# Kernel tuning notes

Hardware: AMD Instinct MI355X
Metric: run time of the kernel (lower is better)

## Reference

```python
import jax, jax.numpy as jnp
import numpy as np

PHI = 0.1  # fraction of pruned weights randomized per inference


def setup_inputs() -> dict:
    key = jax.random.key(0)
    k1, k2, k3 = jax.random.split(key, 3)
    d_out, d_in, batch = 8192, 8192, 256
    W = jax.random.normal(k1, (d_out, d_in), jnp.float32) * 0.02
    prune = jax.random.uniform(k2, (d_out, d_in)) < 0.9
    W = jnp.where(prune, 0.0, W)
    mask = (W == 0.0)  # _register_masks: pruned positions
    x = jax.random.normal(k3, (batch, d_in), jnp.float32)
    return {"x": x, "W": W, "mask": mask}


def reference(x, W, mask):
    # --- _apply_random_flip (vectorized) ---
    n_pruned = int(np.asarray(jnp.sum(mask)))          # concrete mask -> static count
    n_flip = max(1, int(PHI * n_pruned))
    keep = ~mask
    n_keep = jnp.sum(keep).astype(W.dtype)
    wk = jnp.where(keep, W, 0.0)
    mean = jnp.sum(wk) / n_keep
    # torch .std() is unbiased (n-1 denominator)
    var = jnp.sum(jnp.where(keep, (W - mean) ** 2, 0.0)) / (n_keep - 1.0)
    std = jnp.sqrt(var)
    key = jax.random.key(42)
    ks, kv = jax.random.split(key)
    # uniform random permutation of pruned indices -> top_k of random scores
    scores = jnp.where(mask.ravel(), jax.random.uniform(ks, (W.size,)), -1.0)
    _, flip_idx = jax.lax.top_k(scores, n_flip)        # [n_flip] flat indices into W
    vals = jax.random.normal(kv, (n_flip,), W.dtype) * std * 0.1
    W_flipped = W.ravel().at[flip_idx].set(vals).reshape(W.shape)
    # --- base_model forward (Linear, no bias) ---
    out = x @ W_flipped.T                               # [batch, d_out]
    # --- _restore_masks: zero flipped weights again (no effect on out) ---
    _ = jnp.where(mask, 0.0, W_flipped)
    return out
```

## Files before the change

### kernel.cpp

```cpp
#include <hip/hip_runtime.h>

typedef unsigned int u32;
typedef unsigned long long u64;
typedef unsigned short u16;

#define NTOT   67108864u
#define T0P    7543296u
#define PBASE  14733u
#define NSUP   1651u
#define NWSEG  4096u
#define WCAP   2176u
#define RCAP   4352u
#define KSPLIT 8
#define RBLK   512u
#define SEGPB  8

struct Scalars {
  double sumW;
  double sumW2;
  u64 npruned;
  u64 nflip;
  float stdf;
  float pad;
};

#define OFF_COLSUM 0ull
#define OFF_SBASE  8192ull
#define OFF_SC     16384ull
#define OFF_SEGCNT 16512ull
#define OFF_XBF    33024ull
#define OFF_SEGS   4227328ull
#define OFF_ROUTED 39878912ull
#define OFF_WBF    75530496ull
#define WS_NEED_WBF 209748224ull
#define OFF_OUTP   OFF_SEGS

__host__ __device__ inline void tf2x32(u32 k0, u32 k1, u32 x0, u32 x1, u32& y0, u32& y1) {
  u32 ks2 = k0 ^ k1 ^ 0x1BD11BDAu;
  x0 += k0; x1 += k1;
#define TFR(r) { x0 += x1; x1 = (x1 << (r)) | (x1 >> (32 - (r))); x1 ^= x0; }
  TFR(13) TFR(15) TFR(26) TFR(6)  x0 += k1;  x1 += ks2 + 1u;
  TFR(17) TFR(29) TFR(16) TFR(24) x0 += ks2; x1 += k0 + 2u;
  TFR(13) TFR(15) TFR(26) TFR(6)  x0 += k0;  x1 += k1 + 3u;
  TFR(17) TFR(29) TFR(16) TFR(24) x0 += k1;  x1 += ks2 + 4u;
  TFR(13) TFR(15) TFR(26) TFR(6)  x0 += ks2; x1 += k0 + 5u;
#undef TFR
  y0 = x0; y1 = x1;
}

__device__ inline u32 jax_bits32(u32 k0, u32 k1, u32 i) {
  u32 y0, y1; tf2x32(k0, k1, 0u, i, y0, y1);
  return y0 ^ y1;
}

__device__ inline u16 f2bf(float f) {
  union { float f; u32 u; } c; c.f = f;
  u32 r = ((c.u >> 16) & 1u) + 0x7FFFu;
  return (u16)((c.u + r) >> 16);
}

__device__ inline float erfinv32(float x) {
  float w = -log1pf(-x * x);
  float p;
  if (w < 5.0f) {
    w -= 2.5f;
    p = 2.81022636e-08f;
    p = fmaf(p, w, 3.43273939e-07f);
    p = fmaf(p, w, -3.5233877e-06f);
    p = fmaf(p, w, -4.39150654e-06f);
    p = fmaf(p, w, 0.00021858087f);
    p = fmaf(p, w, -0.00125372503f);
    p = fmaf(p, w, -0.00417768164f);
    p = fmaf(p, w, 0.246640727f);
    p = fmaf(p, w, 1.50140941f);
  } else {
    w = sqrtf(w) - 3.0f;
    p = -0.000200214257f;
    p = fmaf(p, w, 0.000100950558f);
    p = fmaf(p, w, 0.00134934322f);
    p = fmaf(p, w, -0.00367342844f);
    p = fmaf(p, w, 0.00573950773f);
    p = fmaf(p, w, -0.0076224613f);
    p = fmaf(p, w, 0.00943887047f);
    p = fmaf(p, w, 1.00167406f);
    p = fmaf(p, w, 2.83297682f);
  }
  return p * x;
}

__global__ __launch_bounds__(256) void k_pass1w(const float* __restrict__ W,
                                                u16* __restrict__ wbf,
                                                const float* __restrict__ x,
                                                u16* __restrict__ xbf,
                                                Scalars* sc, u32* segcnt, u32* segs,
                                                u32 uk0, u32 uk1, u32 dowbf) {
  u32 t = threadIdx.x;
  u32 bid = blockIdx.x;
  if (bid < 1024u) {
    u32 gid = bid * 256 + t;
    u32 lane = t & 63;
    u32 wid = gid >> 6;
    u32* wseg = segs + (u64)wid * WCAP;
    u32 wbase = 0;
    float sf = 0.f, sf2 = 0.f; u32 cnt = 0;
    const u32 stride4 = 1024u * 256u * 4u;
    for (u32 b4 = gid * 4; b4 < NTOT; b4 += stride4) {
      float4 w4 = *(const float4*)(W + b4);
      u32 sb0 = jax_bits32(uk0, uk1, b4 + 0) >> 9;
      u32 sb1 = jax_bits32(uk0, uk1, b4 + 1) >> 9;
      u32 sb2 = jax_bits32(uk0, uk1, b4 + 2) >> 9;
      u32 sb3 = jax_bits32(uk0, uk1, b4 + 3) >> 9;
      float we[4] = {w4.x, w4.y, w4.z, w4.w};
      u32 sbv[4] = {sb0, sb1, sb2, sb3};
      u32 cand[4]; u32 nc = 0;
#pragma unroll
      for (int e = 0; e < 4; e++) {
        float w = we[e];
        sf += w;
        sf2 = fmaf(w, w, sf2);
        bool pr = (w == 0.0f);
        cnt += pr ? 1u : 0u;
        if (pr && sbv[e] >= T0P) { cand[nc] = b4 + e; nc++; }
      }
      u32 inc = nc;
#pragma unroll
      for (int o = 1; o < 64; o <<= 1) { u32 v = (u32)__shfl_up((int)inc, o); if (lane >= (u32)o) inc += v; }
      u32 tot = (u32)__shfl((int)inc, 63);
      u32 pos = wbase + inc - nc;
      for (u32 k2 = 0; k2 < nc; k2++)
        if (pos + k2 < WCAP) wseg[pos + k2] = cand[k2];
      wbase += tot;
    }
    double s = (double)sf, s2 = (double)sf2;
    for (int o = 32; o > 0; o >>= 1) {
      s += __shfl_down(s, o); s2 += __shfl_down(s2, o); cnt += __shfl_down(cnt, o);
    }
    if (lane == 0) {
      atomicAdd(&sc->sumW, s);
      atomicAdd(&sc->sumW2, s2);
      atomicAdd(&sc->npruned, (u64)cnt);
      segcnt[wid] = (wbase > WCAP) ? WCAP : wbase;
    }
  } else if (bid < 1984u) {
    if (!dowbf) return;
    u32 i0 = (bid - 1024u) * 256 + t;
    const u32 stride = 960u * 256u;
    for (u32 g = i0; g < NTOT / 8u; g += stride) {
      const float4* p = (const float4*)(W + (u64)g * 8);
      float4 a = p[0], b = p[1];
      uint4 o;
      o.x = (u32)f2bf(a.x) | ((u32)f2bf(a.y) << 16);
      o.y = (u32)f2bf(a.z) | ((u32)f2bf(a.w) << 16);
      o.z = (u32)f2bf(b.x) | ((u32)f2bf(b.y) << 16);
      o.w = (u32)f2bf(b.z) | ((u32)f2bf(b.w) << 16);
      *(uint4*)(wbf + (u64)g * 8) = o;
    }
  } else {
    u32 i0 = (bid - 1984u) * 256 + t;
    const u32 stride = 64u * 256u;
    for (u32 g = i0; g < 524288u; g += stride) {
      float4 v = ((const float4*)x)[g];
      ushort4 o; o.x = f2bf(v.x); o.y = f2bf(v.y); o.z = f2bf(v.z); o.w = f2bf(v.w);
      ((ushort4*)xbf)[g] = o;
    }
  }
}

__global__ __launch_bounds__(256) void k_route(const u32* __restrict__ segs,
                                               const u32* __restrict__ segcnt,
                                               u32* gcur, u32* routed,
                                               u32 uk0, u32 uk1) {
  __shared__ u32 lhist[2048];
  __shared__ u32 lbase[2048];
  u32 t = threadIdx.x;
  for (u32 j = t; j < 2048; j += 256) lhist[j] = 0;
  __syncthreads();
#pragma unroll 1
  for (int sg = 0; sg < SEGPB; sg++) {
    u32 wid = blockIdx.x * SEGPB + sg;
    u32 n = segcnt[wid]; if (n > WCAP) n = WCAP;
    const u32* sp = segs + (u64)wid * WCAP;
    for (u32 i = t; i < n; i += 256)
      atomicAdd(&lhist[(jax_bits32(uk0, uk1, sp[i]) >> 18) - PBASE], 1u);
  }
  __syncthreads();
  for (u32 j = t; j < 2048; j += 256) {
    u32 c = lhist[j];
    lbase[j] = c ? atomicAdd(&gcur[j], c) : 0u;
    lhist[j] = 0;
  }
  __syncthreads();
#pragma unroll 1
  for (int sg = 0; sg < SEGPB; sg++) {
    u32 wid = blockIdx.x * SEGPB + sg;
    u32 n = segcnt[wid]; if (n > WCAP) n = WCAP;
    const u32* sp = segs + (u64)wid * WCAP;
    for (u32 i = t; i < n; i += 256) {
      u32 idx = sp[i];
      u32 sup = (jax_bits32(uk0, uk1, idx) >> 18) - PBASE;
      u32 pos = lbase[sup] + atomicAdd(&lhist[sup], 1u);
      if (pos < RCAP) routed[(u64)sup * RCAP + pos] = idx;
    }
  }
}

__global__ __launch_bounds__(256) void k_scan(const u32* __restrict__ colsum, Scalars* sc,
                                              u32* sbase) {
  __shared__ u32 h[2048];
  __shared__ u32 wtmp[4];
  u32 t = threadIdx.x, lane = t & 63, wv = t >> 6;
  for (u32 j = t; j < 2048; j += 256) h[j] = colsum[j];
  __syncthreads();
  u32 a[8]; u32 s8 = 0;
#pragma unroll
  for (int k = 0; k < 8; k++) { a[k] = h[2047 - (t * 8 + k)]; s8 += a[k]; }
  u32 inc = s8;
#pragma unroll
  for (int o = 1; o < 64; o <<= 1) { u32 v = (u32)__shfl_up((int)inc, o); if (lane >= (u32)o) inc += v; }
  if (lane == 63) wtmp[wv] = inc;
  __syncthreads();
  u32 woff = 0; for (u32 w = 0; w < wv; w++) woff += wtmp[w];
  u32 base = woff + inc - s8;
#pragma unroll
  for (int k = 0; k < 8; k++) { sbase[2047 - (t * 8 + k)] = base; base += a[k]; }
  if (t == 0) {
    double nk = (double)NTOT - (double)sc->npruned;
    double mean = sc->sumW / nk;
    double var = (sc->sumW2 - 2.0 * mean * sc->sumW + nk * mean * mean) / (nk - 1.0);
    sc->stdf = (float)sqrt(var);
    u64 nfi = (u64)(0.1 * (double)sc->npruned);
    if (nfi < 1) nfi = 1;
    sc->nflip = nfi;
  }
}

__device__ inline void suf512(const u32* cnt, u32* suf, u32* wtmp) {
  u32 t = threadIdx.x, lane = t & 63, wv = t >> 6;
  u32 a0 = cnt[511 - t * 2], a1 = cnt[510 - t * 2];
  u32 s = a0 + a1;
  u32 inc = s;
#pragma unroll
  for (int o = 1; o < 64; o <<= 1) { u32 v = (u32)__shfl_up((int)inc, o); if (lane >= (u32)o) inc += v; }
  if (lane == 63) wtmp[wv] = inc;
  __syncthreads();
  u32 woff = 0;
  for (u32 w = 0; w < wv; w++) woff += wtmp[w];
  u32 base = woff + inc - s;
  suf[511 - t * 2] = base;
  suf[510 - t * 2] = base + a0;
  __syncthreads();
}

template<int MODE>
__global__ __launch_bounds__(256) void k_rank(float* __restrict__ W,
                                              u16* __restrict__ wbf,
                                              const u32* __restrict__ colsum,
                                              const u32* __restrict__ sbase,
                                              const u32* __restrict__ routed,
                                              const Scalars* __restrict__ sc,
                                              u32 uk0, u32 uk1, u32 vk0, u32 vk1) {
  u32 p = blockIdx.x;
  u32 n = colsum[p]; if (n == 0) return;
  if (n > RCAP) n = RCAP;
  u64 nflip = sc->nflip;
  u32 rbase = sbase[p];
  if ((u64)rbase >= nflip) return;
  __shared__ u32 sIdx[RCAP];
  __shared__ u16 sFine[RCAP];
  __shared__ u32 pIdx[RCAP];
  __shared__ u32 hist[512], gbase[512], cur[512], wtmp[4];
  u32 t = threadIdx.x;
  for (u32 j = t; j < 512; j += 256) hist[j] = 0;
  __syncthreads();
  const u32* src = routed + (u64)p * RCAP;
  for (u32 i = t; i < n; i += 256) {
    u32 idx = src[i];
    u32 f = (jax_bits32(uk0, uk1, idx) >> 9) & 511u;
    sIdx[i] = idx;
    sFine[i] = (u16)f;
    atomicAdd(&hist[f], 1u);
  }
  __syncthreads();
  suf512(hist, gbase, wtmp);
  for (u32 j = t; j < 512; j += 256) cur[j] = gbase[j];
  __syncthreads();
  for (u32 i = t; i < n; i += 256) {
    u32 pos = atomicAdd(&cur[sFine[i]], 1u);
    pIdx[pos] = sIdx[i];
  }
  __syncthreads();
  float stdf = sc->stdf;
  for (u32 i = t; i < n; i += 256) {
    u32 f = sFine[i];
    u32 g0 = gbase[f], g1 = g0 + hist[f];
    u32 v = sIdx[i];
    u32 ord = 0;
    for (u32 q = g0; q < g1; q++) ord += (pIdx[q] < v) ? 1u : 0u;
    u64 rank = (u64)rbase + g0 + ord;
    if (rank >= nflip) continue;
    u32 bits = jax_bits32(vk0, vk1, (u32)rank);
    union { u32 u; float fl; } cv; cv.u = 0x3F800000u | (bits >> 9);
    float fu = cv.fl - 1.0f;
    const float lo = -0.99999994f;
    float u2 = fmaxf(lo, fu * 2.0f + lo);
    float nrm = 1.41421354f * erfinv32(u2);
    float val = (nrm * stdf) * 0.1f;
    if (MODE == 1) wbf[v] = f2bf(val);
    else           W[v] = val;
  }
}

typedef __bf16 bf16x8 __attribute__((ext_vector_type(8)));
typedef float f32x4 __attribute__((ext_vector_type(4)));

__global__ __launch_bounds__(256, 3) void k_gemm2(const u16* __restrict__ xbf,
                                                  const u16* __restrict__ wbf,
                                                  float* __restrict__ outp) {
  __shared__ u16 As[128 * 64];
  __shared__ u16 Bs[128 * 64];
  u32 i = blockIdx.x;
  u32 xcd = i & 7u, slot = i >> 3;
  u32 mi = slot & 1u, qq = slot >> 1;
  u32 pid = xcd * 64u + qq;
  u32 kidx = pid >> 6;
  u32 nb = pid & 63u;
  u32 mrow = mi * 128u, nrow = nb * 128u;
  u32 kbase = kidx * 1024u;
  u32 tid = threadIdx.x;
  u32 lane = tid & 63, wv = tid >> 6;
  u32 l8 = lane & 7;
  u32 lr = lane >> 3;
  u32 wm = wv >> 1, wn = wv & 1;
  u32 r = lane & 15, q = lane >> 4;
  f32x4 acc[4][4];
#pragma unroll
  for (int a = 0; a < 4; a++)
#pragma unroll
    for (int b = 0; b < 4; b++) acc[a][b] = (f32x4){0.f, 0.f, 0.f, 0.f};

  for (u32 kb = kbase; kb < kbase + 1024u; kb += 64u) {
#pragma unroll
    for (int j = 0; j < 4; j++) {
      u32 g = wv * 4 + (u32)j;
      u32 row = g * 8 + lr;
      u32 sc = ((l8 ^ (row & 7u)) * 8u);
      const u16* ga = xbf + (u64)(mrow + row) * 8192 + kb + sc;
      __builtin_amdgcn_global_load_lds((const u32*)ga, (u32*)&As[g * 512u], 16, 0, 0);
      const u16* gb = wbf + (u64)(nrow + row) * 8192 + kb + sc;
      __builtin_amdgcn_global_load_lds((const u32*)gb, (u32*)&Bs[g * 512u], 16, 0, 0);
    }
    __syncthreads();
#pragma unroll
    for (int ks = 0; ks < 2; ks++) {
      bf16x8 a[4], b[4];
      u32 ch = (u32)(ks * 4) + q;
#pragma unroll
      for (int mt = 0; mt < 4; mt++) {
        u32 row = wm * 64 + (u32)mt * 16 + r;
        a[mt] = *(bf16x8*)&As[row * 64 + ((ch ^ (r & 7u)) * 8u)];
      }
#pragma unroll
      for (int nt = 0; nt < 4; nt++) {
        u32 row = wn * 64 + (u32)nt * 16 + r;
        b[nt] = *(bf16x8*)&Bs[row * 64 + ((ch ^ (r & 7u)) * 8u)];
      }
#pragma unroll
      for (int mt = 0; mt < 4; mt++)
#pragma unroll
        for (int nt = 0; nt < 4; nt++)
          acc[mt][nt] = __builtin_amdgcn_mfma_f32_16x16x32_bf16(a[mt], b[nt], acc[mt][nt], 0, 0, 0);
    }
    __syncthreads();
  }
  float* op = outp + (u64)kidx * 2097152u;
  u32 quad = lane >> 4, col = lane & 15;
#pragma unroll
  for (int mt = 0; mt < 4; mt++)
#pragma unroll
    for (int nt = 0; nt < 4; nt++) {
      u32 n = nrow + wn * 64 + (u32)nt * 16 + col;
#pragma unroll
      for (int rg = 0; rg < 4; rg++) {
        u32 m = mrow + wm * 64 + (u32)mt * 16 + quad * 4 + (u32)rg;
        op[(u64)m * 8192 + n] = acc[mt][nt][rg];
      }
    }
}

__global__ __launch_bounds__(256) void k_redout(const float* __restrict__ part,
                                                float* __restrict__ out) {
  u32 i = blockIdx.x * 256 + threadIdx.x;
  float4 s = ((const float4*)part)[i];
#pragma unroll
  for (int k = 1; k < KSPLIT; k++) {
    float4 v = ((const float4*)(part + (u64)k * 2097152u))[i];
    s.x += v.x; s.y += v.y; s.z += v.z; s.w += v.w;
  }
  ((float4*)out)[i] = s;
}

__global__ __launch_bounds__(256, 2) void k_gemm_fb(const u16* __restrict__ xbf,
                                                    const float* __restrict__ W,
                                                    float* __restrict__ out) {
  __shared__ u16 xs[256 * 72];
  __shared__ u16 wsm[64 * 72];
  u32 tid = threadIdx.x;
  u32 lane = tid & 63, wv = tid >> 6;
  u32 nt0 = blockIdx.x * 64;
  u32 kbase = blockIdx.y * 2048u;
  f32x4 acc[4][4];
#pragma unroll
  for (int i = 0; i < 4; i++)
#pragma unroll
    for (int j = 0; j < 4; j++) acc[i][j] = (f32x4){0.f, 0.f, 0.f, 0.f};
  for (u32 kb = kbase; kb < kbase + 2048u; kb += 64u) {
#pragma unroll
    for (int r8 = 0; r8 < 8; r8++) {
      u32 row = r8 * 32 + (tid >> 3);
      u32 kseg = (tid & 7) * 8;
      uint4 v = *(const uint4*)(xbf + (u64)row * 8192 + kb + kseg);
      *(uint4*)&xs[row * 72 + kseg] = v;
    }
#pragma unroll
    for (int rr = 0; rr < 4; rr++) {
      u32 f4 = rr * 256 + tid;
      u32 row = f4 >> 4;
      u32 kc = (f4 & 15) * 4;
      float4 v = *(const float4*)(W + (u64)(nt0 + row) * 8192 + kb + kc);
      ushort4 o; o.x = f2bf(v.x); o.y = f2bf(v.y); o.z = f2bf(v.z); o.w = f2bf(v.w);
      *(ushort4*)&wsm[row * 72 + kc] = o;
    }
    __syncthreads();
#pragma unroll
    for (int ks = 0; ks < 2; ks++) {
      bf16x8 a[4], b[4];
      u32 koff = ks * 32 + (lane >> 4) * 8;
      u32 rsel = lane & 15;
#pragma unroll
      for (int mt = 0; mt < 4; mt++) a[mt] = *(bf16x8*)&xs[(wv * 64 + mt * 16 + rsel) * 72 + koff];
#pragma unroll
      for (int nt = 0; nt < 4; nt++) b[nt] = *(bf16x8*)&wsm[(nt * 16 + rsel) * 72 + koff];
#pragma unroll
      for (int mt = 0; mt < 4; mt++)
#pragma unroll
        for (int nt = 0; nt < 4; nt++)
          acc[mt][nt] = __builtin_amdgcn_mfma_f32_16x16x32_bf16(a[mt], b[nt], acc[mt][nt], 0, 0, 0);
    }
    __syncthreads();
  }
  u32 quad = lane >> 4, col = lane & 15;
#pragma unroll
  for (int mt = 0; mt < 4; mt++)
#pragma unroll
    for (int nt = 0; nt < 4; nt++) {
      u32 n = nt0 + nt * 16 + col;
#pragma unroll
      for (int rg = 0; rg < 4; rg++) {
        u32 m = wv * 64 + mt * 16 + quad * 4 + rg;
        atomicAdd(&out[(u64)m * 8192 + n], acc[mt][nt][rg]);
      }
    }
}

extern "C" void kernel_launch(void* const* d_in, const int* in_sizes, int n_in,
                              void* d_out, int out_size, void* d_ws, size_t ws_size,
                              hipStream_t stream) {
  const float* x; float* W;
  if (in_sizes[0] == 2097152) { x = (const float*)d_in[0]; W = (float*)d_in[1]; }
  else                        { x = (const float*)d_in[1]; W = (float*)d_in[0]; }
  float* out = (float*)d_out;
  char* ws = (char*)d_ws;

  u32* colsum = (u32*)(ws + OFF_COLSUM);
  u32* sbase  = (u32*)(ws + OFF_SBASE);
  Scalars* sc = (Scalars*)(ws + OFF_SC);
  u32* segcnt = (u32*)(ws + OFF_SEGCNT);
  u16* xbf    = (u16*)(ws + OFF_XBF);
  u32* segs   = (u32*)(ws + OFF_SEGS);
  u32* routed = (u32*)(ws + OFF_ROUTED);
  u16* wbf    = (u16*)(ws + OFF_WBF);
  float* outp = (float*)(ws + OFF_OUTP);

  bool t1 = (ws_size >= (size_t)WS_NEED_WBF);

  u32 a0, a1, b0, b1;
  tf2x32(0u, 42u, 0u, 0u, a0, a1);
  tf2x32(0u, 42u, 0u, 1u, b0, b1);

  hipMemsetAsync(sc, 0, sizeof(Scalars), stream);
  hipMemsetAsync(colsum, 0, 2048 * sizeof(u32), stream);

  u32 dowbf = t1 ? 1u : 0u;
  k_pass1w<<<2048, 256, 0, stream>>>(W, wbf, x, xbf, sc, segcnt, segs, a0, a1, dowbf);
  k_route<<<RBLK, 256, 0, stream>>>(segs, segcnt, colsum, routed, a0, a1);
  k_scan<<<1, 256, 0, stream>>>(colsum, sc, sbase);
  if (t1) {
    k_rank<1><<<NSUP, 256, 0, stream>>>(W, wbf, colsum, sbase, routed, sc, a0, a1, b0, b1);
    k_gemm2<<<1024, 256, 0, stream>>>(xbf, wbf, outp);
    k_redout<<<2048, 256, 0, stream>>>(outp, out);
  } else {
    k_rank<0><<<NSUP, 256, 0, stream>>>(W, wbf, colsum, sbase, routed, sc, a0, a1, b0, b1);
    hipMemsetAsync(out, 0, (size_t)out_size * 4, stream);
    dim3 g(128, 4);
    k_gemm_fb<<<g, 256, 0, stream>>>(xbf, W, out);
  }
}
```

Before: 965.1 us.

## Bucket-sort flip writes before scattering into bf16 weights; halve GEMM K-split

Instead of scattering the flipped values directly into the bf16 weight copy from k_rank, the new path first writes packed (index, value) records into a flat list. Two new kernels then partition them by high address bits into 1024 buckets and locally sort each bucket before applying, so the final writes to wbf are address-clustered rather than random. Separately, the GEMM K-split drops from 8 to 4, halving the grid and doubling the K loop per block. This adds two launches, extra workspace traffic and needs a larger workspace; if the workspace is too small it falls back to the old path.

```diff
diff --git a/kernel.cpp b/kernel.cpp
--- a/kernel.cpp
+++ b/kernel.cpp
@@ -11,9 +11,12 @@
 #define NWSEG  4096u
 #define WCAP   2176u
 #define RCAP   4352u
-#define KSPLIT 8
+#define KSPLIT 4
 #define RBLK   512u
 #define SEGPB  8
+#define FLIPCAP 6291456u
+#define NBKT   1024u
+#define BCAP1  8192u
 
 struct Scalars {
   double sumW;
@@ -33,6 +36,10 @@
 #define OFF_ROUTED 39878912ull
 #define OFF_WBF    75530496ull
 #define WS_NEED_WBF 209748224ull
+#define OFF_FLIPF  209748224ull
+#define OFF_FB1    260079872ull
+#define OFF_BCUR   327188736ull
+#define WS_NEED_T3 327192832ull
 #define OFF_OUTP   OFF_SEGS
 
 __host__ __device__ inline void tf2x32(u32 k0, u32 k1, u32 x0, u32 x1, u32& y0, u32& y1) {
@@ -254,6 +261,7 @@
 template<int MODE>
 __global__ __launch_bounds__(256) void k_rank(float* __restrict__ W,
                                               u16* __restrict__ wbf,
+                                              u64* __restrict__ flipflat,
                                               const u32* __restrict__ colsum,
                                               const u32* __restrict__ sbase,
                                               const u32* __restrict__ routed,
@@ -305,8 +313,123 @@
     float u2 = fmaxf(lo, fu * 2.0f + lo);
     float nrm = 1.41421354f * erfinv32(u2);
     float val = (nrm * stdf) * 0.1f;
-    if (MODE == 1) wbf[v] = f2bf(val);
-    else           W[v] = val;
+    if (MODE == 2) {
+      if (rank < (u64)FLIPCAP) flipflat[rank] = ((u64)v << 16) | (u64)f2bf(val);
+    } else if (MODE == 1) {
+      wbf[v] = f2bf(val);
+    } else {
+      W[v] = val;
+    }
+  }
+}
+
+__global__ __launch_bounds__(256) void k_part(const u64* __restrict__ flipflat,
+                                              const Scalars* __restrict__ sc,
+                                              u64* __restrict__ fb1,
+                                              u32* __restrict__ bcur) {
+  __shared__ u64 buf[4096];
+  __shared__ u32 hist[1024], pref[1024], base_[1024], cnt2[1024], wtmp[4];
+  u32 t = threadIdx.x, lane = t & 63, wv = t >> 6;
+  u32 nf = (u32)sc->nflip; if (nf > FLIPCAP) nf = FLIPCAP;
+  u32 per = (nf + 255u) / 256u;
+  u32 lo = blockIdx.x * per;
+  u32 hi = lo + per; if (hi > nf) hi = nf;
+  for (u32 c = lo; c < hi; c += 4096u) {
+    u32 m = hi - c; if (m > 4096u) m = 4096u;
+    for (u32 j = t; j < 1024; j += 256) { hist[j] = 0; cnt2[j] = 0; }
+    __syncthreads();
+    u64 it[16];
+#pragma unroll
+    for (int k = 0; k < 16; k++) {
+      u32 i = c + (u32)k * 256u + t;
+      if (i < c + m) { it[k] = flipflat[i]; atomicAdd(&hist[(u32)(it[k] >> 32) & 1023u], 1u); }
+    }
+    __syncthreads();
+    {
+      u32 a4[4]; u32 s4 = 0;
+#pragma unroll
+      for (int k = 0; k < 4; k++) { a4[k] = hist[t * 4 + k]; s4 += a4[k]; }
+      u32 inc = s4;
+#pragma unroll
+      for (int o = 1; o < 64; o <<= 1) { u32 v = (u32)__shfl_up((int)inc, o); if (lane >= (u32)o) inc += v; }
+      if (lane == 63) wtmp[wv] = inc;
+      __syncthreads();
+      u32 woff = 0; for (u32 w = 0; w < wv; w++) woff += wtmp[w];
+      u32 b = woff + inc - s4;
+#pragma unroll
+      for (int k = 0; k < 4; k++) { pref[t * 4 + k] = b; b += a4[k]; }
+    }
+    for (u32 j = t; j < 1024; j += 256) {
+      u32 cc = hist[j];
+      base_[j] = cc ? atomicAdd(&bcur[j], cc) : 0u;
+    }
+    __syncthreads();
+#pragma unroll
+    for (int k = 0; k < 16; k++) {
+      u32 i = c + (u32)k * 256u + t;
+      if (i < c + m) {
+        u32 b = (u32)(it[k] >> 32) & 1023u;
+        u32 p = pref[b] + atomicAdd(&cnt2[b], 1u);
+        buf[p] = it[k];
+      }
+    }
+    __syncthreads();
+    for (u32 j = t; j < m; j += 256) {
+      u64 pk = buf[j];
+      u32 b = (u32)(pk >> 32) & 1023u;
+      u32 pos = base_[b] + (j - pref[b]);
+      if (pos < BCAP1) fb1[(u64)b * BCAP1 + pos] = pk;
+    }
+    __syncthreads();
+  }
+}
+
+__global__ __launch_bounds__(256) void k_apply(const u64* __restrict__ fb1,
+                                               const u32* __restrict__ bcur,
+                                               u16* __restrict__ wbf) {
+  __shared__ u64 buf[4096];
+  __shared__ u32 hist[256], pref[256], cnt2[256], wtmp[4];
+  u32 t = threadIdx.x, lane = t & 63, wv = t >> 6;
+  u32 b = blockIdx.x;
+  u32 n = bcur[b]; if (n > BCAP1) n = BCAP1;
+  const u64* src = fb1 + (u64)b * BCAP1;
+  for (u32 c = 0; c < n; c += 4096u) {
+    u32 m = n - c; if (m > 4096u) m = 4096u;
+    hist[t] = 0; cnt2[t] = 0;
+    __syncthreads();
+    u64 it[16];
+#pragma unroll
+    for (int k = 0; k < 16; k++) {
+      u32 i = c + (u32)k * 256u + t;
+      if (i < c + m) { it[k] = src[i]; atomicAdd(&hist[(u32)(it[k] >> 24) & 255u], 1u); }
+    }
+    __syncthreads();
+    {
+      u32 v0 = hist[t];
+      u32 inc = v0;
+#pragma unroll
+      for (int o = 1; o < 64; o <<= 1) { u32 v = (u32)__shfl_up((int)inc, o); if (lane >= (u32)o) inc += v; }
+      if (lane == 63) wtmp[wv] = inc;
+      __syncthreads();
+      u32 woff = 0; for (u32 w = 0; w < wv; w++) woff += wtmp[w];
+      pref[t] = woff + inc - v0;
+    }
+    __syncthreads();
+#pragma unroll
+    for (int k = 0; k < 16; k++) {
+      u32 i = c + (u32)k * 256u + t;
+      if (i < c + m) {
+        u32 s = (u32)(it[k] >> 24) & 255u;
+        u32 p = pref[s] + atomicAdd(&cnt2[s], 1u);
+        buf[p] = it[k];
+      }
+    }
+    __syncthreads();
+    for (u32 j = t; j < m; j += 256) {
+      u64 pk = buf[j];
+      wbf[(u32)((pk >> 16) & 0x3FFFFFFull)] = (u16)pk;
+    }
+    __syncthreads();
   }
 }
 
@@ -321,11 +444,11 @@
   u32 i = blockIdx.x;
   u32 xcd = i & 7u, slot = i >> 3;
   u32 mi = slot & 1u, qq = slot >> 1;
-  u32 pid = xcd * 64u + qq;
+  u32 pid = xcd * 32u + qq;
   u32 kidx = pid >> 6;
   u32 nb = pid & 63u;
   u32 mrow = mi * 128u, nrow = nb * 128u;
-  u32 kbase = kidx * 1024u;
+  u32 kbase = kidx * 2048u;
   u32 tid = threadIdx.x;
   u32 lane = tid & 63, wv = tid >> 6;
   u32 l8 = lane & 7;
@@ -338,7 +461,7 @@
 #pragma unroll
     for (int b = 0; b < 4; b++) acc[a][b] = (f32x4){0.f, 0.f, 0.f, 0.f};
 
-  for (u32 kb = kbase; kb < kbase + 1024u; kb += 64u) {
+  for (u32 kb = kbase; kb < kbase + 2048u; kb += 64u) {
 #pragma unroll
     for (int j = 0; j < 4; j++) {
       u32 g = wv * 4 + (u32)j;
@@ -480,7 +603,11 @@
   u32* routed = (u32*)(ws + OFF_ROUTED);
   u16* wbf    = (u16*)(ws + OFF_WBF);
   float* outp = (float*)(ws + OFF_OUTP);
-
+  u64* flipflat = (u64*)(ws + OFF_FLIPF);
+  u64* fb1      = (u64*)(ws + OFF_FB1);
+  u32* bcur     = (u32*)(ws + OFF_BCUR);
+
+  bool t3 = (ws_size >= (size_t)WS_NEED_T3);
   bool t1 = (ws_size >= (size_t)WS_NEED_WBF);
 
   u32 a0, a1, b0, b1;
@@ -489,17 +616,24 @@
 
   hipMemsetAsync(sc, 0, sizeof(Scalars), stream);
   hipMemsetAsync(colsum, 0, 2048 * sizeof(u32), stream);
+  if (t3) hipMemsetAsync(bcur, 0, NBKT * sizeof(u32), stream);
 
   u32 dowbf = t1 ? 1u : 0u;
   k_pass1w<<<2048, 256, 0, stream>>>(W, wbf, x, xbf, sc, segcnt, segs, a0, a1, dowbf);
   k_route<<<RBLK, 256, 0, stream>>>(segs, segcnt, colsum, routed, a0, a1);
   k_scan<<<1, 256, 0, stream>>>(colsum, sc, sbase);
-  if (t1) {
-    k_rank<1><<<NSUP, 256, 0, stream>>>(W, wbf, colsum, sbase, routed, sc, a0, a1, b0, b1);
-    k_gemm2<<<1024, 256, 0, stream>>>(xbf, wbf, outp);
+  if (t3) {
+    k_rank<2><<<NSUP, 256, 0, stream>>>(W, wbf, flipflat, colsum, sbase, routed, sc, a0, a1, b0, b1);
+    k_part<<<256, 256, 0, stream>>>(flipflat, sc, fb1, bcur);
+    k_apply<<<NBKT, 256, 0, stream>>>(fb1, bcur, wbf);
+    k_gemm2<<<512, 256, 0, stream>>>(xbf, wbf, outp);
+    k_redout<<<2048, 256, 0, stream>>>(outp, out);
+  } else if (t1) {
+    k_rank<1><<<NSUP, 256, 0, stream>>>(W, wbf, flipflat, colsum, sbase, routed, sc, a0, a1, b0, b1);
+    k_gemm2<<<512, 256, 0, stream>>>(xbf, wbf, outp);
     k_redout<<<2048, 256, 0, stream>>>(outp, out);
   } else {
-    k_rank<0><<<NSUP, 256, 0, stream>>>(W, wbf, colsum, sbase, routed, sc, a0, a1, b0, b1);
+    k_rank<0><<<NSUP, 256, 0, stream>>>(W, wbf, flipflat, colsum, sbase, routed, sc, a0, a1, b0, b1);
     hipMemsetAsync(out, 0, (size_t)out_size * 4, stream);
     dim3 g(128, 4);
     k_gemm_fb<<<g, 256, 0, stream>>>(xbf, W, out);
```

After: 1.074 ms. 1.11x slower.
